# Kernel tuning notes

Measured on AMD Instinct MI355X. Metric: run time of the kernel, lower is better.

The kernel has to match this reference:

```python
import jax, jax.numpy as jnp
import numpy as np

B, L, IN_LEN = 1, 1024, 512
D_MODEL, N_LAYERS = 1024, 4
D_INNER = 2 * D_MODEL
D_STATE = 16
DT_RANK = D_MODEL // 16  # 64
D_CONV = 4
EPS = 1e-5


def setup_inputs() -> dict:
    key = jax.random.key(0)
    ks = jax.random.split(key, 12)
    s = 0.02
    # dt bias init as in mamba_ssm: softplus^{-1}(dt) with dt ~ logUniform(1e-3, 1e-1)
    dt = jnp.exp(jax.random.uniform(ks[7], (N_LAYERS, D_INNER)) * (jnp.log(0.1) - jnp.log(0.001)) + jnp.log(0.001))
    dt_bias = dt + jnp.log(-jnp.expm1(-dt))
    A_log = jnp.log(jnp.broadcast_to(jnp.arange(1, D_STATE + 1, dtype=jnp.float32), (N_LAYERS, D_INNER, D_STATE)))
    return {
        "input": jax.random.normal(ks[0], (B, L, IN_LEN), jnp.float32),
        "inference_parameters": 0,
        "input_w": jax.random.normal(ks[1], (D_MODEL, IN_LEN), jnp.float32) * s,
        "norm_w": jnp.ones((N_LAYERS, D_MODEL), jnp.float32),
        "norm_b": jnp.zeros((N_LAYERS, D_MODEL), jnp.float32),
        "in_proj_w": jax.random.normal(ks[2], (N_LAYERS, 2 * D_INNER, D_MODEL), jnp.float32) * s,
        "conv_w": jax.random.normal(ks[3], (N_LAYERS, D_INNER, D_CONV), jnp.float32) * 0.3,
        "conv_b": jnp.zeros((N_LAYERS, D_INNER), jnp.float32),
        "x_proj_w": jax.random.normal(ks[4], (N_LAYERS, DT_RANK + 2 * D_STATE, D_INNER), jnp.float32) * s,
        "dt_proj_w": jax.random.normal(ks[5], (N_LAYERS, D_INNER, DT_RANK), jnp.float32) * (DT_RANK ** -0.5),
        "dt_proj_b": dt_bias,
        "A_log": A_log,
        "ssm_D": jnp.ones((N_LAYERS, D_INNER), jnp.float32),
        "out_proj_w": jax.random.normal(ks[6], (N_LAYERS, D_MODEL, D_INNER), jnp.float32) * s,
    }


def _layer_norm(x, w, b):
    mu = x.mean(-1, keepdims=True)
    xc = x - mu
    var = (xc * xc).mean(-1, keepdims=True)
    return xc * jax.lax.rsqrt(var + EPS) * w + b


def _mamba(h, ipw, cw, cb, xpw, dtw, dtb, a_log, d_skip, opw):
    # h: [B, L, D_MODEL]
    seqlen = h.shape[1]
    xz = jnp.einsum('bld,ed->ble', h, ipw)  # [B, L, 2*D_INNER]
    x, z = jnp.split(xz, 2, axis=-1)
    # causal depthwise conv1d (kernel D_CONV, left pad D_CONV-1)
    xp = jnp.pad(x, ((0, 0), (D_CONV - 1, 0), (0, 0)))
    x = sum(cw[:, k] * xp[:, k:k + seqlen, :] for k in range(D_CONV)) + cb
    x = jax.nn.silu(x)
    x_dbl = jnp.einsum('bld,ed->ble', x, xpw)  # [B, L, DT_RANK + 2*D_STATE]
    dt = x_dbl[..., :DT_RANK]
    Bc = x_dbl[..., DT_RANK:DT_RANK + D_STATE]  # [B, L, D_STATE]
    Cc = x_dbl[..., DT_RANK + D_STATE:]          # [B, L, D_STATE]
    delta = jax.nn.softplus(jnp.einsum('blr,dr->bld', dt, dtw) + dtb)  # [B, L, D_INNER]
    A = -jnp.exp(a_log)                          # [D_INNER, D_STATE]
    dA = jnp.exp(delta[..., None] * A)           # [B, L, D_INNER, D_STATE]
    dBu = delta[..., None] * Bc[:, :, None, :] * x[..., None]

    def step(hc, t):
        dA_t, dBu_t, C_t = t
        hc = dA_t * hc + dBu_t                   # [B, D_INNER, D_STATE]
        return hc, jnp.einsum('bds,bs->bd', hc, C_t)

    h0 = jnp.zeros((x.shape[0], D_INNER, D_STATE), x.dtype)
    _, ys = jax.lax.scan(step, h0, (dA.transpose(1, 0, 2, 3), dBu.transpose(1, 0, 2, 3), Cc.transpose(1, 0, 2)))
    y = ys.transpose(1, 0, 2) + x * d_skip       # [B, L, D_INNER]
    y = y * jax.nn.silu(z)
    return jnp.einsum('bld,ed->ble', y, opw)     # [B, L, D_MODEL]


def reference(input, inference_parameters, input_w, norm_w, norm_b, in_proj_w, conv_w, conv_b, x_proj_w, dt_proj_w, dt_proj_b, A_log, ssm_D, out_proj_w):
    h = jnp.einsum('bli,di->bld', input, input_w)  # input_layer (no bias)
    res = None
    for i in range(N_LAYERS):
        res = h if res is None else h + res
        hn = _layer_norm(res, norm_w[i], norm_b[i])
        h = _mamba(hn, in_proj_w[i], conv_w[i], conv_b[i], x_proj_w[i], dt_proj_w[i], dt_proj_b[i], A_log[i], ssm_D[i], out_proj_w[i])
    # NOTE: the source forward returns hidden_states directly (norm_f is never applied)
    return h
```

## Files before the change

### kernel.cpp

```cpp
#include <hip/hip_runtime.h>
#include <hip/hip_bf16.h>
#include <math.h>

#define L_SEQ   1024
#define DMODEL  1024
#define DINNER  2048
#define DSTATE  16
#define DTRANK  64
#define NXP     96
#define LN_EPS  1e-5f
#define CHUNK   32
#define NCHUNK  (L_SEQ / CHUNK)
#define SK(l)   ((l) + ((l) >> 5))

typedef __bf16 bf16x8 __attribute__((ext_vector_type(8)));
typedef float  f32x4  __attribute__((ext_vector_type(4)));

__global__ __launch_bounds__(256)
void gemm_bt_bf16(const __hip_bfloat16* __restrict__ A,
                  const __hip_bfloat16* __restrict__ W,
                  float* __restrict__ C,
                  int K, int lda, int ldb, int ldc) {
    __shared__ __hip_bfloat16 As[128][32];
    __shared__ __hip_bfloat16 Bs[128][32];
    const int tid  = threadIdx.x;
    const int lane = tid & 63;
    const int wave = tid >> 6;
    const int m0 = blockIdx.y * 128, n0 = blockIdx.x * 128;
    const int wm = (wave >> 1) * 64, wn = (wave & 1) * 64;
    const int srow = tid >> 2, skcol = (tid & 3) << 3;
    const int fm = lane & 15, fk = (lane >> 4) << 3;

    f32x4 acc[4][4] = {};

    const __hip_bfloat16* Ap0 = A + (size_t)(m0 + srow) * lda + skcol;
    const __hip_bfloat16* Ap1 = Ap0 + (size_t)64 * lda;
    const __hip_bfloat16* Wp0 = W + (size_t)(n0 + srow) * ldb + skcol;
    const __hip_bfloat16* Wp1 = Wp0 + (size_t)64 * ldb;

    for (int k0 = 0; k0 < K; k0 += 32) {
        __syncthreads();
        __builtin_amdgcn_global_load_lds(
            (const __attribute__((address_space(1))) unsigned int*)(Ap0 + k0),
            (__attribute__((address_space(3))) unsigned int*)&As[srow][skcol], 16, 0, 0);
        __builtin_amdgcn_global_load_lds(
            (const __attribute__((address_space(1))) unsigned int*)(Ap1 + k0),
            (__attribute__((address_space(3))) unsigned int*)&As[64 + srow][skcol], 16, 0, 0);
        __builtin_amdgcn_global_load_lds(
            (const __attribute__((address_space(1))) unsigned int*)(Wp0 + k0),
            (__attribute__((address_space(3))) unsigned int*)&Bs[srow][skcol], 16, 0, 0);
        __builtin_amdgcn_global_load_lds(
            (const __attribute__((address_space(1))) unsigned int*)(Wp1 + k0),
            (__attribute__((address_space(3))) unsigned int*)&Bs[64 + srow][skcol], 16, 0, 0);
        __syncthreads();

        bf16x8 af[4], bfr[4];
        #pragma unroll
        for (int i = 0; i < 4; ++i) {
            af[i]  = *(const bf16x8*)&As[wm + i * 16 + fm][fk];
            bfr[i] = *(const bf16x8*)&Bs[wn + i * 16 + fm][fk];
        }
        #pragma unroll
        for (int mt = 0; mt < 4; ++mt)
            #pragma unroll
            for (int nt = 0; nt < 4; ++nt)
                acc[mt][nt] = __builtin_amdgcn_mfma_f32_16x16x32_bf16(
                    af[mt], bfr[nt], acc[mt][nt], 0, 0, 0);
    }

    const int crow = (lane >> 4) << 2;
    const int ccol = lane & 15;
    #pragma unroll
    for (int mt = 0; mt < 4; ++mt)
        #pragma unroll
        for (int nt = 0; nt < 4; ++nt) {
            float* cp = C + (size_t)(m0 + wm + mt * 16 + crow) * ldc
                          + n0 + wn + nt * 16 + ccol;
            #pragma unroll
            for (int r = 0; r < 4; ++r) cp[(size_t)r * ldc] = acc[mt][nt][r];
        }
}

__global__ __launch_bounds__(256)
void gemm_nt(const float* __restrict__ A, const float* __restrict__ W,
             float* __restrict__ C, int M, int N, int K,
             int lda, int ldb, int ldc) {
    __shared__ float As[16][64];
    __shared__ float Bs[16][64];
    const int tid = threadIdx.x;
    const int tx = tid & 15, ty = tid >> 4;
    const int m0 = blockIdx.y * 64, n0 = blockIdx.x * 64;
    const int lr = tid >> 2;
    const int lk = (tid & 3) << 2;
    float acc[4][4] = {};

    for (int k0 = 0; k0 < K; k0 += 16) {
        float4 av = make_float4(0.f, 0.f, 0.f, 0.f);
        float4 bv = make_float4(0.f, 0.f, 0.f, 0.f);
        const int am = m0 + lr;
        if (am < M) av = *(const float4*)(A + (size_t)am * lda + k0 + lk);
        const int bn = n0 + lr;
        if (bn < N) bv = *(const float4*)(W + (size_t)bn * ldb + k0 + lk);
        __syncthreads();
        As[lk + 0][lr] = av.x; As[lk + 1][lr] = av.y;
        As[lk + 2][lr] = av.z; As[lk + 3][lr] = av.w;
        Bs[lk + 0][lr] = bv.x; Bs[lk + 1][lr] = bv.y;
        Bs[lk + 2][lr] = bv.z; Bs[lk + 3][lr] = bv.w;
        __syncthreads();
        #pragma unroll
        for (int k = 0; k < 16; ++k) {
            const float4 a = *(const float4*)&As[k][ty << 2];
            const float4 b = *(const float4*)&Bs[k][tx << 2];
            acc[0][0] += a.x * b.x; acc[0][1] += a.x * b.y;
            acc[0][2] += a.x * b.z; acc[0][3] += a.x * b.w;
            acc[1][0] += a.y * b.x; acc[1][1] += a.y * b.y;
            acc[1][2] += a.y * b.z; acc[1][3] += a.y * b.w;
            acc[2][0] += a.z * b.x; acc[2][1] += a.z * b.y;
            acc[2][2] += a.z * b.z; acc[2][3] += a.z * b.w;
            acc[3][0] += a.w * b.x; acc[3][1] += a.w * b.y;
            acc[3][2] += a.w * b.z; acc[3][3] += a.w * b.w;
        }
    }
    #pragma unroll
    for (int i = 0; i < 4; ++i) {
        const int m = m0 + (ty << 2) + i;
        if (m < M) {
            #pragma unroll
            for (int j = 0; j < 4; ++j) {
                const int n = n0 + (tx << 2) + j;
                if (n < N) C[(size_t)m * ldc + n] = acc[i][j];
            }
        }
    }
}

__global__ __launch_bounds__(256)
void gemm_nn_softplus(const float* __restrict__ A, const float* __restrict__ B,
                      const float* __restrict__ bias, float* __restrict__ C,
                      int K, int lda, int ldb, int ldc) {
    __shared__ float As[16][64];
    __shared__ float Bs[16][64];
    const int t = threadIdx.x;
    const int tx = t & 15, ty = t >> 4;
    const int m0 = blockIdx.y * 64, n0 = blockIdx.x * 64;
    const int ar = t >> 2, ak = (t & 3) << 2;
    const int bk = t >> 4, bn = (t & 15) << 2;
    float acc[4][4] = {};

    for (int k0 = 0; k0 < K; k0 += 16) {
        const float4 av = *(const float4*)(A + (size_t)(m0 + ar) * lda + k0 + ak);
        const float4 bv = *(const float4*)(B + (size_t)(k0 + bk) * ldb + n0 + bn);
        __syncthreads();
        As[ak + 0][ar] = av.x; As[ak + 1][ar] = av.y;
        As[ak + 2][ar] = av.z; As[ak + 3][ar] = av.w;
        *(float4*)&Bs[bk][bn] = bv;
        __syncthreads();
        #pragma unroll
        for (int k = 0; k < 16; ++k) {
            const float4 a = *(const float4*)&As[k][ty << 2];
            const float4 b = *(const float4*)&Bs[k][tx << 2];
            acc[0][0] += a.x * b.x; acc[0][1] += a.x * b.y;
            acc[0][2] += a.x * b.z; acc[0][3] += a.x * b.w;
            acc[1][0] += a.y * b.x; acc[1][1] += a.y * b.y;
            acc[1][2] += a.y * b.z; acc[1][3] += a.y * b.w;
            acc[2][0] += a.z * b.x; acc[2][1] += a.z * b.y;
            acc[2][2] += a.z * b.z; acc[2][3] += a.z * b.w;
            acc[3][0] += a.w * b.x; acc[3][1] += a.w * b.y;
            acc[3][2] += a.w * b.z; acc[3][3] += a.w * b.w;
        }
    }
    #pragma unroll
    for (int i = 0; i < 4; ++i) {
        const int m = m0 + (ty << 2) + i;
        const float bb = bias[m];
        #pragma unroll
        for (int j = 0; j < 4; ++j) {
            const int n = n0 + (tx << 2) + j;
            const float v = acc[i][j] + bb;
            C[(size_t)m * ldc + n] = (v > 20.f) ? v : log1pf(expf(v));
        }
    }
}

__global__ __launch_bounds__(256)
void gemm_nn_splitk(const float* __restrict__ A, const float* __restrict__ B,
                    float* __restrict__ C, int lda, int ldb, int ldc, int kchunk) {
    __shared__ float As[32][32];
    __shared__ float Bs[32][64];
    const int t = threadIdx.x;
    const int tx = t & 15, ty = t >> 4;
    const int m0 = blockIdx.y * 32, n0 = blockIdx.x * 64;
    const int k0s = blockIdx.z * kchunk;
    const int ar = t >> 3, ak = (t & 7) << 2;
    const int bk = t >> 4, bn = (t & 15) << 2;
    float acc[2][4] = {};

    for (int k0 = k0s; k0 < k0s + kchunk; k0 += 32) {
        const float4 av = *(const float4*)(A + (size_t)(m0 + ar) * lda + k0 + ak);
        const float4 bv0 = *(const float4*)(B + (size_t)(k0 + bk) * ldb + n0 + bn);
        const float4 bv1 = *(const float4*)(B + (size_t)(k0 + bk + 16) * ldb + n0 + bn);
        __syncthreads();
        As[ak + 0][ar] = av.x; As[ak + 1][ar] = av.y;
        As[ak + 2][ar] = av.z; As[ak + 3][ar] = av.w;
        *(float4*)&Bs[bk][bn] = bv0;
        *(float4*)&Bs[bk + 16][bn] = bv1;
        __syncthreads();
        #pragma unroll
        for (int k = 0; k < 32; ++k) {
            const float a0 = As[k][(ty << 1) + 0];
            const float a1 = As[k][(ty << 1) + 1];
            const float4 b = *(const float4*)&Bs[k][tx << 2];
            acc[0][0] += a0 * b.x; acc[0][1] += a0 * b.y;
            acc[0][2] += a0 * b.z; acc[0][3] += a0 * b.w;
            acc[1][0] += a1 * b.x; acc[1][1] += a1 * b.y;
            acc[1][2] += a1 * b.z; acc[1][3] += a1 * b.w;
        }
    }
    #pragma unroll
    for (int i = 0; i < 2; ++i) {
        const int m = m0 + (ty << 1) + i;
        #pragma unroll
        for (int j = 0; j < 4; ++j)
            atomicAdd(&C[(size_t)m * ldc + n0 + (tx << 2) + j], acc[i][j]);
    }
}

__global__ __launch_bounds__(256)
void zero_f32(float* __restrict__ p, int n) {
    const int i = blockIdx.x * 256 + threadIdx.x;
    if (i < n) p[i] = 0.f;
}

__global__ __launch_bounds__(256)
void cast_f32_bf16(const float* __restrict__ in, __hip_bfloat16* __restrict__ out,
                   int n4) {
    const int i = blockIdx.x * 256 + threadIdx.x;
    if (i < n4) {
        const float4 v = *(const float4*)(in + (size_t)i * 4);
        __hip_bfloat16 h0 = __float2bfloat16(v.x), h1 = __float2bfloat16(v.y);
        __hip_bfloat16 h2 = __float2bfloat16(v.z), h3 = __float2bfloat16(v.w);
        ushort4 p;
        p.x = *(unsigned short*)&h0; p.y = *(unsigned short*)&h1;
        p.z = *(unsigned short*)&h2; p.w = *(unsigned short*)&h3;
        *(ushort4*)((unsigned short*)out + (size_t)i * 4) = p;
    }
}

__global__ __launch_bounds__(256)
void transpose_bc(const float* __restrict__ xdbl_T, float* __restrict__ xbc) {
    __shared__ float tile[32][33];
    const int t = threadIdx.x;
    const int l0 = blockIdx.x * 32;
    const int s = t >> 3, lc = (t & 7) << 2;
    const float4 v = *(const float4*)(xdbl_T + (size_t)(DTRANK + s) * L_SEQ + l0 + lc);
    tile[s][lc + 0] = v.x; tile[s][lc + 1] = v.y;
    tile[s][lc + 2] = v.z; tile[s][lc + 3] = v.w;
    __syncthreads();
    const int l = t >> 3, sc = (t & 7) << 2;
    float4 w;
    w.x = tile[sc + 0][l]; w.y = tile[sc + 1][l];
    w.z = tile[sc + 2][l]; w.w = tile[sc + 3][l];
    *(float4*)(xbc + (size_t)(l0 + l) * 32 + sc) = w;
}

__global__ __launch_bounds__(256)
void transpose_bf16(const unsigned short* __restrict__ in,
                    unsigned short* __restrict__ out, int R, int Cc) {
    __shared__ unsigned short tile[64][65];
    const int t = threadIdx.x;
    const int r0 = blockIdx.y * 64, c0 = blockIdx.x * 64;
    const int tr = t >> 3, tc8 = (t & 7) << 3;
    #pragma unroll
    for (int i = 0; i < 2; ++i) {
        const int r = tr + i * 32;
        const ushort4 v0 = *(const ushort4*)(in + (size_t)(r0 + r) * Cc + c0 + tc8);
        const ushort4 v1 = *(const ushort4*)(in + (size_t)(r0 + r) * Cc + c0 + tc8 + 4);
        tile[r][tc8 + 0] = v0.x; tile[r][tc8 + 1] = v0.y;
        tile[r][tc8 + 2] = v0.z; tile[r][tc8 + 3] = v0.w;
        tile[r][tc8 + 4] = v1.x; tile[r][tc8 + 5] = v1.y;
        tile[r][tc8 + 6] = v1.z; tile[r][tc8 + 7] = v1.w;
    }
    __syncthreads();
    #pragma unroll
    for (int i = 0; i < 2; ++i) {
        const int r = tr + i * 32;
        ushort4 w0, w1;
        w0.x = tile[tc8 + 0][r]; w0.y = tile[tc8 + 1][r];
        w0.z = tile[tc8 + 2][r]; w0.w = tile[tc8 + 3][r];
        w1.x = tile[tc8 + 4][r]; w1.y = tile[tc8 + 5][r];
        w1.z = tile[tc8 + 6][r]; w1.w = tile[tc8 + 7][r];
        *(ushort4*)(out + (size_t)(c0 + r) * R + r0 + tc8)     = w0;
        *(ushort4*)(out + (size_t)(c0 + r) * R + r0 + tc8 + 4) = w1;
    }
}

__global__ __launch_bounds__(256)
void add_ln(const float* __restrict__ h, float* __restrict__ res,
            __hip_bfloat16* __restrict__ hn, const float* __restrict__ w,
            const float* __restrict__ b, int is_first) {
    const int l = blockIdx.x;
    const int t = threadIdx.x;
    float v[4];
    float s = 0.f, ss = 0.f;
    #pragma unroll
    for (int j = 0; j < 4; ++j) {
        const int d = t + j * 256;
        float x = h[(size_t)l * DMODEL + d];
        if (!is_first) x += res[(size_t)l * DMODEL + d];
        res[(size_t)l * DMODEL + d] = x;
        v[j] = x; s += x; ss += x * x;
    }
    #pragma unroll
    for (int o = 32; o > 0; o >>= 1) {
        s  += __shfl_down(s, o);
        ss += __shfl_down(ss, o);
    }
    __shared__ float sm[4], sm2[4];
    const int wid = t >> 6;
    if ((t & 63) == 0) { sm[wid] = s; sm2[wid] = ss; }
    __syncthreads();
    s  = sm[0] + sm[1] + sm[2] + sm[3];
    ss = sm2[0] + sm2[1] + sm2[2] + sm2[3];
    const float mu  = s * (1.f / DMODEL);
    const float var = ss * (1.f / DMODEL) - mu * mu;
    const float r   = rsqrtf(var + LN_EPS);
    #pragma unroll
    for (int j = 0; j < 4; ++j) {
        const int d = t + j * 256;
        hn[(size_t)l * DMODEL + d] = __float2bfloat16((v[j] - mu) * r * w[d] + b[d]);
    }
}

__global__ __launch_bounds__(256)
void conv_silu_t(const float* __restrict__ xz_T, float* __restrict__ xc_T,
                 const float* __restrict__ cw, const float* __restrict__ cb) {
    const int d = blockIdx.x;
    const int t = threadIdx.x;
    __shared__ float row[L_SEQ];
    *(float4*)&row[t << 2] = *(const float4*)(xz_T + (size_t)d * L_SEQ + (t << 2));
    __syncthreads();
    const float w0 = cw[d * 4 + 0], w1 = cw[d * 4 + 1];
    const float w2 = cw[d * 4 + 2], w3 = cw[d * 4 + 3];
    const float bb = cb[d];
    float o[4];
    #pragma unroll
    for (int j = 0; j < 4; ++j) {
        const int l = (t << 2) + j;
        float acc = bb + w3 * row[l];
        if (l >= 1) acc += w2 * row[l - 1];
        if (l >= 2) acc += w1 * row[l - 2];
        if (l >= 3) acc += w0 * row[l - 3];
        const float sig = 1.f / (1.f + __expf(-acc));
        o[j] = acc * sig;
    }
    *(float4*)(xc_T + (size_t)d * L_SEQ + (t << 2)) = make_float4(o[0], o[1], o[2], o[3]);
}

__global__ __launch_bounds__(512)
void ssm_scan_t(const float* __restrict__ delta_T,
                const float* __restrict__ xc_T,
                const float* __restrict__ xbc,
                const float* __restrict__ xz_T,
                const float* __restrict__ alog,
                const float* __restrict__ dsk,
                __hip_bfloat16* __restrict__ y_T) {
    const int d = blockIdx.x;
    const int t = threadIdx.x;
    const int s = t & 15;
    const int c = t >> 4;

    __shared__ float sdl[L_SEQ + 32], sxl[L_SEQ + 32];
    __shared__ float sz[L_SEQ], sy[L_SEQ];
    __shared__ float saprod[NCHUNK][DSTATE];
    __shared__ float shloc[NCHUNK][DSTATE];
    __shared__ float shstart[NCHUNK][DSTATE];

    if (t < 256) {
        const float4 v = ((const float4*)(delta_T + (size_t)d * L_SEQ))[t];
        const int l = t << 2;
        sdl[SK(l)] = v.x; sdl[SK(l + 1)] = v.y;
        sdl[SK(l + 2)] = v.z; sdl[SK(l + 3)] = v.w;
        ((float4*)sz)[t] = ((const float4*)(xz_T + (size_t)(DINNER + d) * L_SEQ))[t];
    } else {
        const int tt = t - 256;
        const float4 v = ((const float4*)(xc_T + (size_t)d * L_SEQ))[tt];
        const int l = tt << 2;
        sxl[SK(l)] = v.x; sxl[SK(l + 1)] = v.y;
        sxl[SK(l + 2)] = v.z; sxl[SK(l + 3)] = v.w;
    }
    __syncthreads();

    const float A  = -expf(alog[d * DSTATE + s]);
    const int   l0 = c * CHUNK;

    float aprod = 1.f, h = 0.f;
    #pragma unroll 4
    for (int j = 0; j < CHUNK; ++j) {
        const int l = l0 + j;
        const float dl = sdl[SK(l)];
        const float da = __expf(dl * A);
        h = da * h + dl * xbc[(size_t)l * 32 + s] * sxl[SK(l)];
        aprod *= da;
    }
    saprod[c][s] = aprod;
    shloc[c][s]  = h;
    __syncthreads();

    if (c == 0) {
        float hs = 0.f;
        for (int cc = 0; cc < NCHUNK; ++cc) {
            shstart[cc][s] = hs;
            hs = saprod[cc][s] * hs + shloc[cc][s];
        }
    }
    __syncthreads();

    h = shstart[c][s];
    const float Dk = dsk[d];
    #pragma unroll 4
    for (int j = 0; j < CHUNK; ++j) {
        const int l = l0 + j;
        const float dl = sdl[SK(l)];
        const float xl = sxl[SK(l)];
        h = __expf(dl * A) * h + dl * xbc[(size_t)l * 32 + s] * xl;
        float cch = h * xbc[(size_t)l * 32 + 16 + s];
        cch += __shfl_xor(cch, 1, 16);
        cch += __shfl_xor(cch, 2, 16);
        cch += __shfl_xor(cch, 4, 16);
        cch += __shfl_xor(cch, 8, 16);
        if (s == 0) {
            const float zl  = sz[l];
            const float sig = 1.f / (1.f + __expf(-zl));
            sy[l] = (cch + xl * Dk) * (zl * sig);
        }
    }
    __syncthreads();

    if (t < 256) {
        const float4 v = ((const float4*)sy)[t];
        __hip_bfloat16 h0 = __float2bfloat16(v.x), h1 = __float2bfloat16(v.y);
        __hip_bfloat16 h2 = __float2bfloat16(v.z), h3 = __float2bfloat16(v.w);
        ushort4 p;
        p.x = *(unsigned short*)&h0; p.y = *(unsigned short*)&h1;
        p.z = *(unsigned short*)&h2; p.w = *(unsigned short*)&h3;
        *(ushort4*)((unsigned short*)y_T + (size_t)d * L_SEQ + (t << 2)) = p;
    }
}

extern "C" void kernel_launch(void* const* d_in, const int* in_sizes, int n_in,
                              void* d_out, int out_size, void* d_ws, size_t ws_size,
                              hipStream_t stream) {
    const float* input   = (const float*)d_in[0];
    const float* input_w = (const float*)d_in[2];
    const float* norm_w  = (const float*)d_in[3];
    const float* norm_b  = (const float*)d_in[4];
    const float* ipw     = (const float*)d_in[5];
    const float* cw      = (const float*)d_in[6];
    const float* cb      = (const float*)d_in[7];
    const float* xpw     = (const float*)d_in[8];
    const float* dtw     = (const float*)d_in[9];
    const float* dtb     = (const float*)d_in[10];
    const float* alog    = (const float*)d_in[11];
    const float* dsk     = (const float*)d_in[12];
    const float* opw     = (const float*)d_in[13];
    float* out = (float*)d_out;

    float* ws      = (float*)d_ws;
    float* h       = ws;
    float* res     = h       + (1u << 20);
    float* xz_T    = res     + (1u << 20);
    float* xc_T    = xz_T    + (4u << 20);
    float* xdbl_T  = xc_T    + (2u << 20);
    float* xbc     = xdbl_T  + (NXP * L_SEQ);
    float* delta_T = xbc     + (L_SEQ * 32);
    __hip_bfloat16* hn_bf  = (__hip_bfloat16*)(delta_T + (2u << 20));
    __hip_bfloat16* yT_bf  = hn_bf  + (1u << 20);
    __hip_bfloat16* y_bf   = yT_bf  + (2u << 20);
    __hip_bfloat16* ipw_bf = y_bf   + (2u << 20);
    __hip_bfloat16* opw_bf = ipw_bf + (4u << 20);

    const dim3 blk(256);

    gemm_nt<<<dim3(DMODEL / 64, L_SEQ / 64), blk, 0, stream>>>(
        input, input_w, h, L_SEQ, DMODEL, 512, 512, 512, DMODEL);

    for (int i = 0; i < 4; ++i) {
        cast_f32_bf16<<<(2 * DINNER * DMODEL / 4 + 255) / 256, blk, 0, stream>>>(
            ipw + (size_t)i * 2 * DINNER * DMODEL, ipw_bf, 2 * DINNER * DMODEL / 4);

        add_ln<<<L_SEQ, 256, 0, stream>>>(
            h, res, hn_bf, norm_w + i * DMODEL, norm_b + i * DMODEL, i == 0);

        gemm_bt_bf16<<<dim3(L_SEQ / 128, 2 * DINNER / 128), blk, 0, stream>>>(
            ipw_bf, hn_bf, xz_T, DMODEL, DMODEL, DMODEL, L_SEQ);

        conv_silu_t<<<DINNER, 256, 0, stream>>>(
            xz_T, xc_T, cw + i * DINNER * 4, cb + i * DINNER);

        zero_f32<<<(NXP * L_SEQ + 255) / 256, blk, 0, stream>>>(xdbl_T, NXP * L_SEQ);
        gemm_nn_splitk<<<dim3(L_SEQ / 64, 3, 8), blk, 0, stream>>>(
            xpw + (size_t)i * NXP * DINNER, xc_T, xdbl_T,
            DINNER, L_SEQ, L_SEQ, DINNER / 8);

        transpose_bc<<<L_SEQ / 32, 256, 0, stream>>>(xdbl_T, xbc);

        gemm_nn_softplus<<<dim3(L_SEQ / 64, DINNER / 64), blk, 0, stream>>>(
            dtw + (size_t)i * DINNER * DTRANK, xdbl_T, dtb + i * DINNER, delta_T,
            DTRANK, DTRANK, L_SEQ, L_SEQ);

        ssm_scan_t<<<DINNER, 512, 0, stream>>>(
            delta_T, xc_T, xbc, xz_T,
            alog + i * DINNER * DSTATE, dsk + i * DINNER, yT_bf);

        transpose_bf16<<<dim3(L_SEQ / 64, DINNER / 64), blk, 0, stream>>>(
            (const unsigned short*)yT_bf, (unsigned short*)y_bf, DINNER, L_SEQ);

        cast_f32_bf16<<<(DMODEL * DINNER / 4 + 255) / 256, blk, 0, stream>>>(
            opw + (size_t)i * DMODEL * DINNER, opw_bf, DMODEL * DINNER / 4);
        float* dst = (i == 3) ? out : h;
        gemm_bt_bf16<<<dim3(DMODEL / 128, L_SEQ / 128), blk, 0, stream>>>(
            y_bf, opw_bf, dst, DINNER, DINNER, DINNER, DMODEL);
    }
}
```

Before: 906.1 us.

## Split-K bf16 GEMMs with atomics, merge cast/zero kernels, reuse scan prefix state

Both bf16 MFMA GEMMs now split K across blockIdx.z: two ways for in_proj and four for out_proj. Partial results are accumulated with atomicAdd, so the small out_proj grid gets enough blocks to fill the CUs. A combined zero kernel clears xdbl, xz_T and the output buffer ahead of the atomics, and the two weight casts are merged into one launch. The SSM scan keeps the per-step cumulative decay and local state in registers, so the second pass becomes a single FMA instead of recomputing exp. The cost is extra atomic and zeroing memory traffic, plus register pressure from the unrolled 32-entry arrays.

```diff
diff --git a/kernel.cpp b/kernel.cpp
--- a/kernel.cpp
+++ b/kernel.cpp
@@ -17,16 +17,17 @@
 typedef float  f32x4  __attribute__((ext_vector_type(4)));
 
 __global__ __launch_bounds__(256)
-void gemm_bt_bf16(const __hip_bfloat16* __restrict__ A,
-                  const __hip_bfloat16* __restrict__ W,
-                  float* __restrict__ C,
-                  int K, int lda, int ldb, int ldc) {
+void gemm_bt_bf16_sk(const __hip_bfloat16* __restrict__ A,
+                     const __hip_bfloat16* __restrict__ W,
+                     float* __restrict__ C,
+                     int kchunk, int lda, int ldb, int ldc) {
     __shared__ __hip_bfloat16 As[128][32];
     __shared__ __hip_bfloat16 Bs[128][32];
     const int tid  = threadIdx.x;
     const int lane = tid & 63;
     const int wave = tid >> 6;
     const int m0 = blockIdx.y * 128, n0 = blockIdx.x * 128;
+    const int k0s = blockIdx.z * kchunk;
     const int wm = (wave >> 1) * 64, wn = (wave & 1) * 64;
     const int srow = tid >> 2, skcol = (tid & 3) << 3;
     const int fm = lane & 15, fk = (lane >> 4) << 3;
@@ -38,7 +39,7 @@
     const __hip_bfloat16* Wp0 = W + (size_t)(n0 + srow) * ldb + skcol;
     const __hip_bfloat16* Wp1 = Wp0 + (size_t)64 * ldb;
 
-    for (int k0 = 0; k0 < K; k0 += 32) {
+    for (int k0 = k0s; k0 < k0s + kchunk; k0 += 32) {
         __syncthreads();
         __builtin_amdgcn_global_load_lds(
             (const __attribute__((address_space(1))) unsigned int*)(Ap0 + k0),
@@ -77,7 +78,8 @@
             float* cp = C + (size_t)(m0 + wm + mt * 16 + crow) * ldc
                           + n0 + wn + nt * 16 + ccol;
             #pragma unroll
-            for (int r = 0; r < 4; ++r) cp[(size_t)r * ldc] = acc[mt][nt][r];
+            for (int r = 0; r < 4; ++r)
+                atomicAdd(&cp[(size_t)r * ldc], acc[mt][nt][r]);
         }
 }
 
@@ -226,24 +228,31 @@
 }
 
 __global__ __launch_bounds__(256)
-void zero_f32(float* __restrict__ p, int n) {
+void zero3(float* __restrict__ a, int na, float* __restrict__ b, int nb,
+           float* __restrict__ c2, int nc) {
     const int i = blockIdx.x * 256 + threadIdx.x;
-    if (i < n) p[i] = 0.f;
-}
-
-__global__ __launch_bounds__(256)
-void cast_f32_bf16(const float* __restrict__ in, __hip_bfloat16* __restrict__ out,
-                   int n4) {
-    const int i = blockIdx.x * 256 + threadIdx.x;
-    if (i < n4) {
-        const float4 v = *(const float4*)(in + (size_t)i * 4);
-        __hip_bfloat16 h0 = __float2bfloat16(v.x), h1 = __float2bfloat16(v.y);
-        __hip_bfloat16 h2 = __float2bfloat16(v.z), h3 = __float2bfloat16(v.w);
-        ushort4 p;
-        p.x = *(unsigned short*)&h0; p.y = *(unsigned short*)&h1;
-        p.z = *(unsigned short*)&h2; p.w = *(unsigned short*)&h3;
-        *(ushort4*)((unsigned short*)out + (size_t)i * 4) = p;
-    }
+    if (i < na) a[i] = 0.f;
+    else if (i < na + nb) b[i - na] = 0.f;
+    else if (i < na + nb + nc) c2[i - na - nb] = 0.f;
+}
+
+__global__ __launch_bounds__(256)
+void cast_weights(const float* __restrict__ ina, __hip_bfloat16* __restrict__ outa,
+                  int n4a, const float* __restrict__ inb,
+                  __hip_bfloat16* __restrict__ outb, int n4b) {
+    int i = blockIdx.x * 256 + threadIdx.x;
+    const float* in;
+    __hip_bfloat16* out;
+    if (i < n4a) { in = ina; out = outa; }
+    else if (i < n4a + n4b) { in = inb; out = outb; i -= n4a; }
+    else return;
+    const float4 v = *(const float4*)(in + (size_t)i * 4);
+    __hip_bfloat16 h0 = __float2bfloat16(v.x), h1 = __float2bfloat16(v.y);
+    __hip_bfloat16 h2 = __float2bfloat16(v.z), h3 = __float2bfloat16(v.w);
+    ushort4 p;
+    p.x = *(unsigned short*)&h0; p.y = *(unsigned short*)&h1;
+    p.z = *(unsigned short*)&h2; p.w = *(unsigned short*)&h3;
+    *(ushort4*)((unsigned short*)out + (size_t)i * 4) = p;
 }
 
 __global__ __launch_bounds__(256)
@@ -356,7 +365,7 @@
     *(float4*)(xc_T + (size_t)d * L_SEQ + (t << 2)) = make_float4(o[0], o[1], o[2], o[3]);
 }
 
-__global__ __launch_bounds__(512)
+__global__ __launch_bounds__(512, 4)
 void ssm_scan_t(const float* __restrict__ delta_T,
                 const float* __restrict__ xc_T,
                 const float* __restrict__ xbc,
@@ -393,14 +402,16 @@
     const float A  = -expf(alog[d * DSTATE + s]);
     const int   l0 = c * CHUNK;
 
+    float ap[CHUNK], hl[CHUNK];
     float aprod = 1.f, h = 0.f;
-    #pragma unroll 4
+    #pragma unroll
     for (int j = 0; j < CHUNK; ++j) {
         const int l = l0 + j;
         const float dl = sdl[SK(l)];
         const float da = __expf(dl * A);
         h = da * h + dl * xbc[(size_t)l * 32 + s] * sxl[SK(l)];
         aprod *= da;
+        ap[j] = aprod; hl[j] = h;
     }
     saprod[c][s] = aprod;
     shloc[c][s]  = h;
@@ -415,20 +426,19 @@
     }
     __syncthreads();
 
-    h = shstart[c][s];
+    const float h0 = shstart[c][s];
     const float Dk = dsk[d];
-    #pragma unroll 4
+    #pragma unroll
     for (int j = 0; j < CHUNK; ++j) {
         const int l = l0 + j;
-        const float dl = sdl[SK(l)];
-        const float xl = sxl[SK(l)];
-        h = __expf(dl * A) * h + dl * xbc[(size_t)l * 32 + s] * xl;
-        float cch = h * xbc[(size_t)l * 32 + 16 + s];
+        const float hj = fmaf(h0, ap[j], hl[j]);
+        float cch = hj * xbc[(size_t)l * 32 + 16 + s];
         cch += __shfl_xor(cch, 1, 16);
         cch += __shfl_xor(cch, 2, 16);
         cch += __shfl_xor(cch, 4, 16);
         cch += __shfl_xor(cch, 8, 16);
         if (s == 0) {
+            const float xl  = sxl[SK(l)];
             const float zl  = sz[l];
             const float sig = 1.f / (1.f + __expf(-zl));
             sy[l] = (cch + xl * Dk) * (zl * sig);
@@ -438,11 +448,11 @@
 
     if (t < 256) {
         const float4 v = ((const float4*)sy)[t];
-        __hip_bfloat16 h0 = __float2bfloat16(v.x), h1 = __float2bfloat16(v.y);
-        __hip_bfloat16 h2 = __float2bfloat16(v.z), h3 = __float2bfloat16(v.w);
+        __hip_bfloat16 h0b = __float2bfloat16(v.x), h1b = __float2bfloat16(v.y);
+        __hip_bfloat16 h2b = __float2bfloat16(v.z), h3b = __float2bfloat16(v.w);
         ushort4 p;
-        p.x = *(unsigned short*)&h0; p.y = *(unsigned short*)&h1;
-        p.z = *(unsigned short*)&h2; p.w = *(unsigned short*)&h3;
+        p.x = *(unsigned short*)&h0b; p.y = *(unsigned short*)&h1b;
+        p.z = *(unsigned short*)&h2b; p.w = *(unsigned short*)&h3b;
         *(ushort4*)((unsigned short*)y_T + (size_t)d * L_SEQ + (t << 2)) = p;
     }
 }
@@ -480,24 +490,31 @@
     __hip_bfloat16* opw_bf = ipw_bf + (4u << 20);
 
     const dim3 blk(256);
+    const int n4_ipw = 2 * DINNER * DMODEL / 4;
+    const int n4_opw = DMODEL * DINNER / 4;
+    const int nz = NXP * L_SEQ + L_SEQ * DMODEL + 2 * DINNER * L_SEQ;
 
     gemm_nt<<<dim3(DMODEL / 64, L_SEQ / 64), blk, 0, stream>>>(
         input, input_w, h, L_SEQ, DMODEL, 512, 512, 512, DMODEL);
 
     for (int i = 0; i < 4; ++i) {
-        cast_f32_bf16<<<(2 * DINNER * DMODEL / 4 + 255) / 256, blk, 0, stream>>>(
-            ipw + (size_t)i * 2 * DINNER * DMODEL, ipw_bf, 2 * DINNER * DMODEL / 4);
+        cast_weights<<<(n4_ipw + n4_opw + 255) / 256, blk, 0, stream>>>(
+            ipw + (size_t)i * 2 * DINNER * DMODEL, ipw_bf, n4_ipw,
+            opw + (size_t)i * DMODEL * DINNER, opw_bf, n4_opw);
 
         add_ln<<<L_SEQ, 256, 0, stream>>>(
             h, res, hn_bf, norm_w + i * DMODEL, norm_b + i * DMODEL, i == 0);
 
-        gemm_bt_bf16<<<dim3(L_SEQ / 128, 2 * DINNER / 128), blk, 0, stream>>>(
-            ipw_bf, hn_bf, xz_T, DMODEL, DMODEL, DMODEL, L_SEQ);
+        float* dst = (i == 3) ? out : h;
+        zero3<<<(nz + 255) / 256, blk, 0, stream>>>(
+            xdbl_T, NXP * L_SEQ, dst, L_SEQ * DMODEL, xz_T, 2 * DINNER * L_SEQ);
+
+        gemm_bt_bf16_sk<<<dim3(L_SEQ / 128, 2 * DINNER / 128, 2), blk, 0, stream>>>(
+            ipw_bf, hn_bf, xz_T, DMODEL / 2, DMODEL, DMODEL, L_SEQ);
 
         conv_silu_t<<<DINNER, 256, 0, stream>>>(
             xz_T, xc_T, cw + i * DINNER * 4, cb + i * DINNER);
 
-        zero_f32<<<(NXP * L_SEQ + 255) / 256, blk, 0, stream>>>(xdbl_T, NXP * L_SEQ);
         gemm_nn_splitk<<<dim3(L_SEQ / 64, 3, 8), blk, 0, stream>>>(
             xpw + (size_t)i * NXP * DINNER, xc_T, xdbl_T,
             DINNER, L_SEQ, L_SEQ, DINNER / 8);
@@ -515,10 +532,7 @@
         transpose_bf16<<<dim3(L_SEQ / 64, DINNER / 64), blk, 0, stream>>>(
             (const unsigned short*)yT_bf, (unsigned short*)y_bf, DINNER, L_SEQ);
 
-        cast_f32_bf16<<<(DMODEL * DINNER / 4 + 255) / 256, blk, 0, stream>>>(
-            opw + (size_t)i * DMODEL * DINNER, opw_bf, DMODEL * DINNER / 4);
-        float* dst = (i == 3) ? out : h;
-        gemm_bt_bf16<<<dim3(DMODEL / 128, L_SEQ / 128), blk, 0, stream>>>(
-            y_bf, opw_bf, dst, DINNER, DINNER, DINNER, DMODEL);
-    }
-}
+        gemm_bt_bf16_sk<<<dim3(DMODEL / 128, L_SEQ / 128, 4), blk, 0, stream>>>(
+            y_bf, opw_bf, dst, DINNER / 4, DINNER, DINNER, DMODEL);
+    }
+}
```

After: 922.9 us. Within noise of the previous version (+1.9%).
